# Kernel tuning notes

Measured on AMD Instinct MI355X. Metric: run time of the kernel, lower is better.

## Reference

```python
import jax, jax.numpy as jnp
import numpy as np

DIM, NH = 256, 8
B, L_INNER, L_LEAF, L_ROOT = 16, 128, 64, 16


def mha(q, k, v, wi, bi, wo, bo, nh=NH):
    # Faithful torch.nn.MultiheadAttention (batch_first): packed in_proj, q scaled by head_dim**-0.5.
    E = q.shape[-1]
    hd = E // nh
    wq, wk, wv = wi[:E], wi[E:2 * E], wi[2 * E:]
    bq, bk, bv = bi[:E], bi[E:2 * E], bi[2 * E:]

    def proj(x, w, b):
        Bx, Lx, _ = x.shape
        return (x @ w.T + b).reshape(Bx, Lx, nh, hd).transpose(0, 2, 1, 3)  # [B,H,L,hd]

    qh = proj(q, wq, bq) * (float(hd) ** -0.5)
    kh = proj(k, wk, bk)
    vh = proj(v, wv, bv)
    attn = jax.nn.softmax(jnp.einsum('bhqd,bhkd->bhqk', qh, kh), axis=-1)
    o = jnp.einsum('bhqk,bhkd->bhqd', attn, vh).transpose(0, 2, 1, 3).reshape(q.shape)
    return o @ wo.T + bo


def setup_inputs() -> dict:
    key = jax.random.key(0)
    ks = jax.random.split(key, 10)
    return {
        'leaf': jax.random.normal(ks[0], (B * L_INNER, L_LEAF, DIM), jnp.float32),
        'inner': jax.random.normal(ks[1], (B, L_INNER, DIM), jnp.float32),
        'root': jax.random.normal(ks[2], (B, L_ROOT, DIM), jnp.float32),
        'w_in': jax.random.normal(ks[3], (7, 3 * DIM, DIM), jnp.float32) * 0.02,
        'b_in': jax.random.normal(ks[4], (7, 3 * DIM), jnp.float32) * 0.02,
        'w_out': jax.random.normal(ks[5], (7, DIM, DIM), jnp.float32) * 0.02,
        'b_out': jax.random.normal(ks[6], (7, DIM), jnp.float32) * 0.02,
        'weight_leaf': jax.random.normal(ks[7], (2,), jnp.float32),
        'weight_inner': jax.random.normal(ks[8], (3,), jnp.float32),
        'weight_root': jax.random.normal(ks[9], (2,), jnp.float32),
    }


def reference(leaf, inner, root, w_in, b_in, w_out, b_out, weight_leaf, weight_inner, weight_root):
    # param slots: 0 leaf_parents, 1 leaf_siblings, 2 inner_parents, 3 inner_siblings,
    #              4 inner_children, 5 root_siblings, 6 root_children (constructed but UNUSED, as in source)
    inner_flat = inner.reshape(-1, 1, DIM)  # [B*L_inner, 1, dim]

    leaf_p = mha(leaf, inner_flat, inner_flat, w_in[0], b_in[0], w_out[0], b_out[0])
    leaf_s = mha(leaf, leaf, leaf, w_in[1], b_in[1], w_out[1], b_out[1])
    wl = jax.nn.softmax(weight_leaf)
    leaf_out = wl[0] * leaf_p + wl[1] * leaf_s

    inner_p = mha(inner, root, root, w_in[2], b_in[2], w_out[2], b_out[2])
    inner_s = mha(inner, inner, inner, w_in[3], b_in[3], w_out[3], b_out[3])
    inner_c = mha(inner_flat, leaf, leaf, w_in[4], b_in[4], w_out[4], b_out[4]).reshape(inner.shape)
    wi_ = jax.nn.softmax(weight_inner)
    inner_out = wi_[0] * inner_p + wi_[1] * inner_s + wi_[2] * inner_c

    root_s = mha(root, root, root, w_in[5], b_in[5], w_out[5], b_out[5])
    # source bug reproduced: root_c also uses attn_root_siblings (slot 5)
    root_c = mha(root, inner, inner, w_in[5], b_in[5], w_out[5], b_out[5])
    wr = jax.nn.softmax(weight_root)
    root_out = wr[0] * root_s + wr[1] * root_c

    return (leaf_out, inner_out, root_out)
```

## Files before the change

### kernel.cpp

```cpp
#include <hip/hip_runtime.h>
#include <hip/hip_bf16.h>
#include <cstdint>


#define DIM 256
#define NH 8
#define HD 32

static constexpr float SCALE = 0.17677669529663687f;

typedef __bf16 bf16x8 __attribute__((ext_vector_type(8)));
typedef __bf16 bf16x4 __attribute__((ext_vector_type(4)));
typedef float  f32x4  __attribute__((ext_vector_type(4)));

__device__ __forceinline__ float dot4(const float4 a, const float4 b) {
    return a.x * b.x + a.y * b.y + a.z * b.z + a.w * b.w;
}

__global__ __launch_bounds__(256) void cvt_f2b(const float* __restrict__ s,
                                               __bf16* __restrict__ d, int n) {
    int i = (blockIdx.x * 256 + threadIdx.x) * 4;
    if (i < n) {
        float4 v = *(const float4*)(s + i);
        d[i + 0] = (__bf16)v.x; d[i + 1] = (__bf16)v.y;
        d[i + 2] = (__bf16)v.z; d[i + 3] = (__bf16)v.w;
    }
}

__device__ void mega2_body(int g,
    const float* __restrict__ X, const float* __restrict__ inner,
    const __bf16* __restrict__ W1b, const float* __restrict__ Bi1,
    const __bf16* __restrict__ W4kvb, const float* __restrict__ W4q,
    const float* __restrict__ Bi4, __bf16* __restrict__ O1,
    float* __restrict__ Oc, char* __restrict__ smem)
{
    const int xcd  = g & 7;
    const int idx  = g >> 3;
    const int b    = xcd * 256 + (idx >> 2);
    const int hg   = idx & 3;
    const int tid  = threadIdx.x;
    const int wid  = tid >> 6;
    const int lane = tid & 63;
    const int lr   = lane & 15;
    const int lk   = (lane >> 4) * 8;
    const int prow = (lane >> 4) * 4;
    const int tok0 = wid * 16 + prow;

    __bf16* Qs  = (__bf16*)smem;
    __bf16* Ks  = (__bf16*)(smem + 9216);
    __bf16* Vt  = (__bf16*)(smem + 18432);
    __bf16* K4t = (__bf16*)(smem + 27648);
    __bf16* V4t = (__bf16*)(smem + 36864);
    __bf16* Pw  = (__bf16*)(smem + 46080 + wid * 2304);
    float* qpart = (float*)(smem + 55296);
    float* qv    = qpart + 256;
    float* psm   = qv + 64;
    float* opart = psm + 128;
    __bf16* Bs  = (__bf16*)(smem + 57600);

    bf16x8 a[8];
    {
        const float* xrow = X + ((size_t)b * 64 + wid * 16 + lr) * DIM + lk;
#pragma unroll
        for (int k = 0; k < 8; ++k) {
            float4 v0 = *(const float4*)(xrow + k * 32);
            float4 v1 = *(const float4*)(xrow + k * 32 + 4);
            bf16x8 t;
            t[0] = (__bf16)v0.x; t[1] = (__bf16)v0.y; t[2] = (__bf16)v0.z; t[3] = (__bf16)v0.w;
            t[4] = (__bf16)v1.x; t[5] = (__bf16)v1.y; t[6] = (__bf16)v1.z; t[7] = (__bf16)v1.w;
            a[k] = t;
        }
    }

    {
        const int srow = tid >> 5;
        const int scol = (tid & 31) * 8;
        auto wsrc = [&](int t) -> const __bf16* {
            if (t < 12) {
                const int sec = t >> 2, sub = t & 3;
                return W1b + (size_t)(sec * 256 + hg * 64 + sub * 16) * DIM;
            }
            const int u = t - 12, sec = u >> 2, sub = u & 3;
            return W4kvb + (size_t)(sec * 256 + hg * 64 + sub * 16) * DIM;
        };
        {
            const __bf16* p = wsrc(0);
            bf16x8 g0 = *(const bf16x8*)(p + (size_t)srow * DIM + scol);
            bf16x8 g1 = *(const bf16x8*)(p + (size_t)(8 + srow) * DIM + scol);
            *(bf16x8*)(Bs + srow * 264 + scol) = g0;
            *(bf16x8*)(Bs + (8 + srow) * 264 + scol) = g1;
        }
        __syncthreads();

        for (int t = 0; t < 20; ++t) {
            const int cur = t & 1;
            const __bf16* Bc = Bs + cur * 4224;
            bf16x8 g0, g1;
            if (t + 1 < 20) {
                const __bf16* p = wsrc(t + 1);
                g0 = *(const bf16x8*)(p + (size_t)srow * DIM + scol);
                g1 = *(const bf16x8*)(p + (size_t)(8 + srow) * DIM + scol);
            }
            f32x4 aL = {0.f, 0.f, 0.f, 0.f}, aH = {0.f, 0.f, 0.f, 0.f};
#pragma unroll
            for (int kk = 0; kk < 4; ++kk) {
                const bf16x8 bL = *(const bf16x8*)(Bc + lr * 264 + kk * 32 + lk);
                aL = __builtin_amdgcn_mfma_f32_16x16x32_bf16(a[kk], bL, aL, 0, 0, 0);
            }
#pragma unroll
            for (int kk = 0; kk < 4; ++kk) {
                const bf16x8 bH = *(const bf16x8*)(Bc + lr * 264 + (kk + 4) * 32 + lk);
                aH = __builtin_amdgcn_mfma_f32_16x16x32_bf16(a[kk + 4], bH, aH, 0, 0, 0);
            }
            const f32x4 acc = aL + aH;
            const int sub = t & 3;
            const int col = sub * 16 + lr;
            if (t < 4) {
                const float bias = Bi1[hg * 64 + sub * 16 + lr];
#pragma unroll
                for (int r = 0; r < 4; ++r)
                    Qs[(size_t)(tok0 + r) * 72 + col] = (__bf16)((acc[r] + bias) * SCALE);
            } else if (t < 8) {
                const float bias = Bi1[256 + hg * 64 + sub * 16 + lr];
#pragma unroll
                for (int r = 0; r < 4; ++r)
                    Ks[(size_t)(tok0 + r) * 72 + col] = (__bf16)(acc[r] + bias);
            } else {
                bf16x4 pv;
                if (t < 12) {
                    const float bias = Bi1[512 + hg * 64 + sub * 16 + lr];
#pragma unroll
                    for (int r = 0; r < 4; ++r) pv[r] = (__bf16)(acc[r] + bias);
                    *(bf16x4*)(Vt + (size_t)col * 72 + tok0) = pv;
                } else if (t < 16) {
                    const float bias = Bi4[256 + hg * 64 + sub * 16 + lr];
#pragma unroll
                    for (int r = 0; r < 4; ++r) pv[r] = (__bf16)(acc[r] + bias);
                    *(bf16x4*)(K4t + (size_t)col * 72 + tok0) = pv;
                } else {
                    const float bias = Bi4[512 + hg * 64 + sub * 16 + lr];
#pragma unroll
                    for (int r = 0; r < 4; ++r) pv[r] = (__bf16)(acc[r] + bias);
                    *(bf16x4*)(V4t + (size_t)col * 72 + tok0) = pv;
                }
            }
            if (t + 1 < 20) {
                __bf16* Bn = Bs + (cur ^ 1) * 4224;
                *(bf16x8*)(Bn + srow * 264 + scol) = g0;
                *(bf16x8*)(Bn + (8 + srow) * 264 + scol) = g1;
            }
            __syncthreads();
        }
    }

    {
        const int o = tid & 63, part = tid >> 6;
        const float4* wr = (const float4*)(W4q + (size_t)(hg * 64 + o) * DIM + part * 64);
        const float4* xr = (const float4*)(inner + (size_t)b * DIM + part * 64);
        float accq = 0.f;
#pragma unroll
        for (int k = 0; k < 16; ++k) accq += dot4(xr[k], wr[k]);
        qpart[part * 64 + o] = accq;
    }
    __syncthreads();

    if (tid < 64)
        qv[tid] = (qpart[tid] + qpart[64 + tid] + qpart[128 + tid] + qpart[192 + tid]
                   + Bi4[hg * 64 + tid]) * SCALE;

    const int hh = wid >> 1;
    const int qh = wid & 1;
    f32x4 s[2][4];
    {
        bf16x8 kb[4];
#pragma unroll
        for (int kt = 0; kt < 4; ++kt)
            kb[kt] = *(const bf16x8*)(Ks + (size_t)(kt * 16 + lr) * 72 + hh * 32 + lk);
#pragma unroll
        for (int q2 = 0; q2 < 2; ++q2) {
            const int qt = qh * 2 + q2;
            const bf16x8 qa = *(const bf16x8*)(Qs + (size_t)(qt * 16 + lr) * 72 + hh * 32 + lk);
#pragma unroll
            for (int kt = 0; kt < 4; ++kt) {
                f32x4 z = {0.f, 0.f, 0.f, 0.f};
                s[q2][kt] = __builtin_amdgcn_mfma_f32_16x16x32_bf16(qa, kb[kt], z, 0, 0, 0);
            }
        }
    }
#pragma unroll
    for (int q2 = 0; q2 < 2; ++q2) {
#pragma unroll
        for (int r = 0; r < 4; ++r) {
            float m = fmaxf(fmaxf(s[q2][0][r], s[q2][1][r]), fmaxf(s[q2][2][r], s[q2][3][r]));
#pragma unroll
            for (int off = 1; off < 16; off <<= 1) m = fmaxf(m, __shfl_xor(m, off));
            const float p0 = __expf(s[q2][0][r] - m), p1 = __expf(s[q2][1][r] - m);
            const float p2 = __expf(s[q2][2][r] - m), p3 = __expf(s[q2][3][r] - m);
            float t = p0 + p1 + p2 + p3;
#pragma unroll
            for (int off = 1; off < 16; off <<= 1) t += __shfl_xor(t, off);
            const float inv = 1.0f / t;
            s[q2][0][r] = p0 * inv; s[q2][1][r] = p1 * inv;
            s[q2][2][r] = p2 * inv; s[q2][3][r] = p3 * inv;
        }
    }
    {
        bf16x8 vb[2][2];
#pragma unroll
        for (int dt = 0; dt < 2; ++dt)
#pragma unroll
            for (int ks = 0; ks < 2; ++ks)
                vb[dt][ks] = *(const bf16x8*)(Vt + (size_t)(hh * 32 + dt * 16 + lr) * 72 + ks * 32 + lk);
#pragma unroll
        for (int q2 = 0; q2 < 2; ++q2) {
            const int qt = qh * 2 + q2;
#pragma unroll
            for (int kt = 0; kt < 4; ++kt)
#pragma unroll
                for (int r = 0; r < 4; ++r)
                    Pw[(size_t)(prow + r) * 72 + kt * 16 + lr] = (__bf16)s[q2][kt][r];
            bf16x8 pa[2];
#pragma unroll
            for (int ks = 0; ks < 2; ++ks)
                pa[ks] = *(const bf16x8*)(Pw + (size_t)lr * 72 + ks * 32 + lk);
#pragma unroll
            for (int dt = 0; dt < 2; ++dt) {
                f32x4 o = {0.f, 0.f, 0.f, 0.f};
#pragma unroll
                for (int ks = 0; ks < 2; ++ks)
                    o = __builtin_amdgcn_mfma_f32_16x16x32_bf16(pa[ks], vb[dt][ks], o, 0, 0, 0);
                const int colO = (hg * 2 + hh) * 32 + dt * 16 + lr;
#pragma unroll
                for (int r = 0; r < 4; ++r)
                    O1[((size_t)b * 64 + qt * 16 + prow + r) * DIM + colO] = (__bf16)o[r];
            }
        }
    }
    __syncthreads();

    if (wid < 2) {
        const int j = lane;
        float sv = 0.f;
#pragma unroll
        for (int d = 0; d < 32; ++d)
            sv += qv[wid * 32 + d] * (float)K4t[(size_t)(wid * 32 + d) * 72 + j];
        float m = sv;
#pragma unroll
        for (int off = 1; off < 64; off <<= 1) m = fmaxf(m, __shfl_xor(m, off));
        const float p = __expf(sv - m);
        float t = p;
#pragma unroll
        for (int off = 1; off < 64; off <<= 1) t += __shfl_xor(t, off);
        psm[wid * 64 + j] = p / t;
    }
    __syncthreads();

    if (tid < 128) {
        const int o = tid & 63, hf = tid >> 6;
        const int ho = o >> 5;
        float acc2 = 0.f;
#pragma unroll
        for (int j = 0; j < 32; ++j)
            acc2 += psm[ho * 64 + hf * 32 + j] * (float)V4t[(size_t)o * 72 + hf * 32 + j];
        opart[hf * 64 + o] = acc2;
    }
    __syncthreads();
    if (tid < 64)
        Oc[(size_t)b * DIM + hg * 64 + tid] = opart[tid] + opart[64 + tid];
}

__device__ void leafp_mfma_body(int bid, const float* __restrict__ inner,
    const __bf16* __restrict__ Wv0b, const __bf16* __restrict__ Wo0b,
    const float* __restrict__ b_in0, const float* __restrict__ b_out0,
    float* __restrict__ tP, char* __restrict__ smem)
{
    __bf16* tV = (__bf16*)smem;
    __bf16* Bs = (__bf16*)(smem + 33792);
    const int tid  = threadIdx.x;
    const int wid  = tid >> 6;
    const int lane = tid & 63;
    const int lr   = lane & 15;
    const int lk   = (lane >> 4) * 8;
    const int prow = (lane >> 4) * 4;
    const int tok0 = wid * 16 + prow;
    const int srow = tid >> 5;
    const int scol = (tid & 31) * 8;

    bf16x8 a[8];
    {
        const float* xrow = inner + ((size_t)bid * 64 + wid * 16 + lr) * DIM + lk;
#pragma unroll
        for (int k = 0; k < 8; ++k) {
            float4 v0 = *(const float4*)(xrow + k * 32);
            float4 v1 = *(const float4*)(xrow + k * 32 + 4);
            bf16x8 t;
            t[0] = (__bf16)v0.x; t[1] = (__bf16)v0.y; t[2] = (__bf16)v0.z; t[3] = (__bf16)v0.w;
            t[4] = (__bf16)v1.x; t[5] = (__bf16)v1.y; t[6] = (__bf16)v1.z; t[7] = (__bf16)v1.w;
            a[k] = t;
        }
    }

    {
        bf16x8 g0 = *(const bf16x8*)(Wv0b + (size_t)srow * DIM + scol);
        bf16x8 g1 = *(const bf16x8*)(Wv0b + (size_t)(8 + srow) * DIM + scol);
        *(bf16x8*)(Bs + srow * 264 + scol) = g0;
        *(bf16x8*)(Bs + (8 + srow) * 264 + scol) = g1;
    }
    __syncthreads();
    for (int t = 0; t < 16; ++t) {
        const int cur = t & 1;
        const __bf16* Bc = Bs + cur * 4224;
        bf16x8 g0, g1;
        if (t + 1 < 16) {
            const __bf16* p = Wv0b + (size_t)((t + 1) * 16) * DIM;
            g0 = *(const bf16x8*)(p + (size_t)srow * DIM + scol);
            g1 = *(const bf16x8*)(p + (size_t)(8 + srow) * DIM + scol);
        }
        f32x4 acc = {0.f, 0.f, 0.f, 0.f};
#pragma unroll
        for (int k = 0; k < 8; ++k)
            acc = __builtin_amdgcn_mfma_f32_16x16x32_bf16(
                a[k], *(const bf16x8*)(Bc + lr * 264 + k * 32 + lk), acc, 0, 0, 0);
        const float bias = b_in0[512 + t * 16 + lr];
#pragma unroll
        for (int r = 0; r < 4; ++r)
            tV[(size_t)(tok0 + r) * 264 + t * 16 + lr] = (__bf16)(acc[r] + bias);
        if (t + 1 < 16) {
            __bf16* Bn = Bs + (cur ^ 1) * 4224;
            *(bf16x8*)(Bn + srow * 264 + scol) = g0;
            *(bf16x8*)(Bn + (8 + srow) * 264 + scol) = g1;
        }
        __syncthreads();
    }

    bf16x8 a2[8];
#pragma unroll
    for (int k = 0; k < 8; ++k)
        a2[k] = *(const bf16x8*)(tV + (size_t)(wid * 16 + lr) * 264 + k * 32 + lk);
    {
        bf16x8 g0 = *(const bf16x8*)(Wo0b + (size_t)srow * DIM + scol);
        bf16x8 g1 = *(const bf16x8*)(Wo0b + (size_t)(8 + srow) * DIM + scol);
        *(bf16x8*)(Bs + srow * 264 + scol) = g0;
        *(bf16x8*)(Bs + (8 + srow) * 264 + scol) = g1;
    }
    __syncthreads();
    for (int t = 0; t < 16; ++t) {
        const int cur = t & 1;
        const __bf16* Bc = Bs + cur * 4224;
        bf16x8 g0, g1;
        if (t + 1 < 16) {
            const __bf16* p = Wo0b + (size_t)((t + 1) * 16) * DIM;
            g0 = *(const bf16x8*)(p + (size_t)srow * DIM + scol);
            g1 = *(const bf16x8*)(p + (size_t)(8 + srow) * DIM + scol);
        }
        f32x4 acc = {0.f, 0.f, 0.f, 0.f};
#pragma unroll
        for (int k = 0; k < 8; ++k)
            acc = __builtin_amdgcn_mfma_f32_16x16x32_bf16(
                a2[k], *(const bf16x8*)(Bc + lr * 264 + k * 32 + lk), acc, 0, 0, 0);
        const float bo = b_out0[t * 16 + lr];
#pragma unroll
        for (int r = 0; r < 4; ++r)
            tP[((size_t)bid * 64 + wid * 16 + prow + r) * DIM + t * 16 + lr] = acc[r] + bo;
        if (t + 1 < 16) {
            __bf16* Bn = Bs + (cur ^ 1) * 4224;
            *(bf16x8*)(Bn + srow * 264 + scol) = g0;
            *(bf16x8*)(Bn + (8 + srow) * 264 + scol) = g1;
        }
        __syncthreads();
    }
}

template <int LQ, int LK, int RQ>
__device__ void attn_body(int bx, const float* __restrict__ Xq,
                          const float* __restrict__ Xkv,
                          const float* __restrict__ Wi, const float* __restrict__ Bi,
                          float* __restrict__ O, float* __restrict__ sm)
{
    const int b   = bx >> 3;
    const int h   = bx & 7;
    const int tid = threadIdx.x;

    float* KsP = sm;
    float* VsP = KsP + LK * 33;
    float* QsP = VsP + LK * 33;
    float* SP  = QsP + LQ * 33;

    const float* xq  = Xq  + (size_t)b * LQ * DIM;
    const float* xkv = Xkv + (size_t)b * LK * DIM;

    {
        const int col   = tid & 63;
        const int which = col >> 5;
        const int d     = col & 31;
        const int row   = DIM + which * DIM + h * HD + d;
        const float4* wr = (const float4*)(Wi + (size_t)row * DIM);
        const float bias = Bi[row];
        constexpr int TT = LK / 4;
        float acc[TT];
#pragma unroll
        for (int i = 0; i < TT; ++i) acc[i] = 0.f;
        const int t0 = tid >> 6;
        for (int k4 = 0; k4 < DIM / 4; ++k4) {
            const float4 w = wr[k4];
#pragma unroll
            for (int i = 0; i < TT; ++i) {
                const int t = t0 + 4 * i;
                const float4 aa = ((const float4*)(xkv + (size_t)t * DIM))[k4];
                acc[i] += dot4(aa, w);
            }
        }
#pragma unroll
        for (int i = 0; i < TT; ++i) {
            const int t = t0 + 4 * i;
            if (which == 0) KsP[t * 33 + d] = acc[i] + bias;
            else            VsP[t * 33 + d] = acc[i] + bias;
        }
    }
    {
        constexpr int TGQ = (LQ >= 8) ? 8 : LQ;
        constexpr int TT  = LQ / TGQ;
        if (tid < 32 * TGQ) {
            const int d   = tid & 31;
            const int row = h * HD + d;
            const float4* wr = (const float4*)(Wi + (size_t)row * DIM);
            const float bias = Bi[row];
            float acc[TT];
#pragma unroll
            for (int i = 0; i < TT; ++i) acc[i] = 0.f;
            const int t0 = tid >> 5;
            for (int k4 = 0; k4 < DIM / 4; ++k4) {
                const float4 w = wr[k4];
#pragma unroll
                for (int i = 0; i < TT; ++i) {
                    const int t = t0 + TGQ * i;
                    const float4 aa = ((const float4*)(xq + (size_t)t * DIM))[k4];
                    acc[i] += dot4(aa, w);
                }
            }
#pragma unroll
            for (int i = 0; i < TT; ++i) {
                const int t = t0 + TGQ * i;
                QsP[t * 33 + d] = (acc[i] + bias) * SCALE;
            }
        }
    }
    __syncthreads();

    for (int q0 = 0; q0 < LQ; q0 += RQ) {
        for (int idx = tid; idx < RQ * LK; idx += 256) {
            const int r = idx / LK;
            const int j = idx - r * LK;
            float acc = 0.f;
#pragma unroll
            for (int d = 0; d < HD; ++d)
                acc += QsP[(q0 + r) * 33 + d] * KsP[j * 33 + d];
            SP[r * (LK + 1) + j] = acc;
        }
        __syncthreads();
        if (tid < RQ * 8) {
            const int r   = tid >> 3;
            const int sub = tid & 7;
            float m = -1e30f;
            for (int j = sub; j < LK; j += 8) m = fmaxf(m, SP[r * (LK + 1) + j]);
#pragma unroll
            for (int off = 4; off; off >>= 1) m = fmaxf(m, __shfl_xor(m, off, 8));
            float sum = 0.f;
            for (int j = sub; j < LK; j += 8) {
                const float p = __expf(SP[r * (LK + 1) + j] - m);
                SP[r * (LK + 1) + j] = p;
                sum += p;
            }
#pragma unroll
            for (int off = 4; off; off >>= 1) sum += __shfl_xor(sum, off, 8);
            const float inv = 1.0f / sum;
            for (int j = sub; j < LK; j += 8) SP[r * (LK + 1) + j] *= inv;
        }
        __syncthreads();
        for (int idx = tid; idx < RQ * HD; idx += 256) {
            const int r = idx >> 5;
            const int d = idx & 31;
            float acc = 0.f;
            for (int j = 0; j < LK; ++j)
                acc += SP[r * (LK + 1) + j] * VsP[j * 33 + d];
            O[((size_t)(b * LQ + q0 + r)) * DIM + h * HD + d] = acc;
        }
        __syncthreads();
    }
}

__global__ __launch_bounds__(256, 2) void fused_main(
    const float* __restrict__ leaf, const float* __restrict__ inner,
    const float* __restrict__ root,
    const float* __restrict__ w_in, const float* __restrict__ b_in,
    const float* __restrict__ b_out,
    const __bf16* __restrict__ W1b, const __bf16* __restrict__ W4kvb,
    const __bf16* __restrict__ Wv0b, const __bf16* __restrict__ Wo0b,
    __bf16* __restrict__ O1, float* __restrict__ Oc, float* __restrict__ tP,
    float* __restrict__ Op, float* __restrict__ Osf,
    float* __restrict__ Ors, float* __restrict__ Orc)
{
    extern __shared__ __align__(16) char smem[];
    const int bid = blockIdx.x;
    const size_t WI = 768 * 256, BI = 768;
    if (bid < 128)
        attn_body<128, 128, 16>(bid, inner, inner, w_in + 3 * WI, b_in + 3 * BI,
                                Osf, (float*)smem);
    else if (bid < 256)
        attn_body<128, 16, 32>(bid - 128, inner, root, w_in + 2 * WI, b_in + 2 * BI,
                               Op, (float*)smem);
    else if (bid < 384)
        attn_body<16, 128, 16>(bid - 256, root, inner, w_in + 5 * WI, b_in + 5 * BI,
                               Orc, (float*)smem);
    else if (bid < 512)
        attn_body<16, 16, 16>(bid - 384, root, root, w_in + 5 * WI, b_in + 5 * BI,
                              Ors, (float*)smem);
    else if (bid < 544)
        leafp_mfma_body(bid - 512, inner, Wv0b, Wo0b, b_in, b_out, tP, smem);
    else
        mega2_body(bid - 544, leaf, inner, W1b, b_in + 1 * BI, W4kvb,
                   w_in + 4 * WI, b_in + 4 * BI, O1, Oc, smem);
}

__device__ void combleaf_body(int bid, const __bf16* __restrict__ O1,
                              const __bf16* __restrict__ Wob,
                              const float* __restrict__ Bo1,
                              const float* __restrict__ tP,
                              const float* __restrict__ wleaf,
                              float* __restrict__ out, char* __restrict__ sm)
{
    const int tid  = threadIdx.x;
    const int wid  = tid >> 6;
    const int lane = tid & 63;
    const int lr   = lane & 15;
    const int lk   = (lane >> 4) * 8;
    __bf16* Bs = (__bf16*)sm;
    const int srow = tid >> 5;
    const int scol = (tid & 31) * 8;

    bf16x8 a[8];
    {
        const __bf16* ar = O1 + ((size_t)bid * 64 + wid * 16 + lr) * DIM + lk;
#pragma unroll
        for (int k = 0; k < 8; ++k) a[k] = *(const bf16x8*)(ar + k * 32);
    }
    const float e0 = __expf(wleaf[0]), e1 = __expf(wleaf[1]);
    const float wl0 = e0 / (e0 + e1), wl1 = e1 / (e0 + e1);
    const size_t row0 = (size_t)bid * 64 + wid * 16 + (lane >> 4) * 4;

    {
        bf16x8 g0 = *(const bf16x8*)(Wob + (size_t)srow * DIM + scol);
        bf16x8 g1 = *(const bf16x8*)(Wob + (size_t)(8 + srow) * DIM + scol);
        *(bf16x8*)(Bs + srow * 264 + scol) = g0;
        *(bf16x8*)(Bs + (8 + srow) * 264 + scol) = g1;
    }
    __syncthreads();

    for (int nt = 0; nt < 16; ++nt) {
        const int cur = nt & 1;
        const __bf16* Bc = Bs + cur * 4224;
        bf16x8 g0, g1;
        if (nt + 1 < 16) {
            const __bf16* p = Wob + (size_t)((nt + 1) * 16) * DIM;
            g0 = *(const bf16x8*)(p + (size_t)srow * DIM + scol);
            g1 = *(const bf16x8*)(p + (size_t)(8 + srow) * DIM + scol);
        }
        f32x4 acc = {0.f, 0.f, 0.f, 0.f};
#pragma unroll
        for (int k = 0; k < 8; ++k)
            acc = __builtin_amdgcn_mfma_f32_16x16x32_bf16(
                a[k], *(const bf16x8*)(Bc + lr * 264 + k * 32 + lk), acc, 0, 0, 0);
        const int   o  = nt * 16 + lr;
        const float bo = Bo1[o];
        const float tv = tP[(size_t)bid * DIM + o];
#pragma unroll
        for (int r = 0; r < 4; ++r)
            out[(row0 + r) * DIM + o] = wl0 * tv + wl1 * (acc[r] + bo);
        if (nt + 1 < 16) {
            __bf16* Bn = Bs + (cur ^ 1) * 4224;
            *(bf16x8*)(Bn + srow * 264 + scol) = g0;
            *(bf16x8*)(Bn + (8 + srow) * 264 + scol) = g1;
        }
        __syncthreads();
    }
}

__device__ void combine_inner_body(int vb, const float* __restrict__ Op,
    const float* __restrict__ Osf, const float* __restrict__ Oc,
    const float* __restrict__ W2, const float* __restrict__ B2,
    const float* __restrict__ W3, const float* __restrict__ B3,
    const float* __restrict__ W4, const float* __restrict__ B4,
    const float* __restrict__ winner, float* __restrict__ out, float* __restrict__ Ts)
{
    const int n0 = vb * 32;
    const int o  = threadIdx.x;
    const float e0 = __expf(winner[0]), e1 = __expf(winner[1]), e2 = __expf(winner[2]);
    const float inv = 1.f / (e0 + e1 + e2);
    const float wt0 = e0 * inv, wt1 = e1 * inv, wt2 = e2 * inv;

    float acc[32];
#pragma unroll
    for (int r = 0; r < 32; ++r) acc[r] = 0.f;
    const float biasacc = wt0 * B2[o] + wt1 * B3[o] + wt2 * B4[o];

#pragma unroll
    for (int term = 0; term < 3; ++term) {
        const float* Ob = (term == 0) ? Op : (term == 1) ? Osf : Oc;
        const float* Wb = (term == 0) ? W2 : (term == 1) ? W3 : W4;
        const float wt  = (term == 0) ? wt0 : (term == 1) ? wt1 : wt2;
        __syncthreads();
        for (int idx = threadIdx.x; idx < 32 * DIM; idx += 256)
            Ts[idx] = Ob[(size_t)n0 * DIM + idx];
        __syncthreads();
        const float4* wr = (const float4*)(Wb + (size_t)o * DIM);
        for (int k4 = 0; k4 < DIM / 4; ++k4) {
            float4 w = wr[k4];
            w.x *= wt; w.y *= wt; w.z *= wt; w.w *= wt;
#pragma unroll
            for (int r = 0; r < 32; ++r) {
                const float4 aa = *(const float4*)&Ts[r * DIM + k4 * 4];
                acc[r] += dot4(aa, w);
            }
        }
    }
#pragma unroll
    for (int r = 0; r < 32; ++r)
        out[(size_t)(n0 + r) * DIM + o] = acc[r] + biasacc;
}

__device__ void combine_root_body(int vb, const float* __restrict__ Ors,
    const float* __restrict__ Orc, const float* __restrict__ W5,
    const float* __restrict__ B5, const float* __restrict__ wroot,
    float* __restrict__ out, float* __restrict__ Ts)
{
    const int n0 = vb * 32;
    const int o  = threadIdx.x;
    const float e0 = __expf(wroot[0]), e1 = __expf(wroot[1]);
    const float w0 = e0 / (e0 + e1), w1 = e1 / (e0 + e1);
    for (int idx = threadIdx.x; idx < 32 * DIM; idx += 256)
        Ts[idx] = w0 * Ors[(size_t)n0 * DIM + idx] + w1 * Orc[(size_t)n0 * DIM + idx];
    __syncthreads();
    float acc[32];
#pragma unroll
    for (int r = 0; r < 32; ++r) acc[r] = 0.f;
    const float4* wr = (const float4*)(W5 + (size_t)o * DIM);
    for (int k4 = 0; k4 < DIM / 4; ++k4) {
        const float4 w = wr[k4];
#pragma unroll
        for (int r = 0; r < 32; ++r) {
            const float4 aa = *(const float4*)&Ts[r * DIM + k4 * 4];
            acc[r] += dot4(aa, w);
        }
    }
    const float bo = B5[o];
#pragma unroll
    for (int r = 0; r < 32; ++r)
        out[(size_t)(n0 + r) * DIM + o] = acc[r] + bo;
}

__global__ __launch_bounds__(256) void epilogue_kernel(
    const __bf16* __restrict__ O1, const __bf16* __restrict__ Wo1b,
    const float* __restrict__ w_out, const float* __restrict__ b_out,
    const float* __restrict__ tP, const float* __restrict__ Op,
    const float* __restrict__ Osf, const float* __restrict__ Oc,
    const float* __restrict__ Ors, const float* __restrict__ Orc,
    const float* __restrict__ wleaf, const float* __restrict__ winner,
    const float* __restrict__ wroot, float* __restrict__ out)
{
    extern __shared__ float smf[];
    const int bid = blockIdx.x;
    const size_t WO = 256 * 256, BO = 256;
    if (bid < 2048)
        combleaf_body(bid, O1, Wo1b, b_out + BO, tP, wleaf, out, (char*)smf);
    else if (bid < 2112)
        combine_inner_body(bid - 2048, Op, Osf, Oc,
                           w_out + 2 * WO, b_out + 2 * BO,
                           w_out + 3 * WO, b_out + 3 * BO,
                           w_out + 4 * WO, b_out + 4 * BO,
                           winner, out + 33554432, smf);
    else
        combine_root_body(bid - 2112, Ors, Orc, w_out + 5 * WO, b_out + 5 * BO,
                          wroot, out + 33554432 + 524288, smf);
}

extern "C" void kernel_launch(void* const* d_in, const int* in_sizes, int n_in,
                              void* d_out, int out_size, void* d_ws, size_t ws_size,
                              hipStream_t stream)
{
    const float* leaf   = (const float*)d_in[0];
    const float* inner  = (const float*)d_in[1];
    const float* root   = (const float*)d_in[2];
    const float* w_in   = (const float*)d_in[3];
    const float* b_in   = (const float*)d_in[4];
    const float* w_out  = (const float*)d_in[5];
    const float* b_out  = (const float*)d_in[6];
    const float* wleaf  = (const float*)d_in[7];
    const float* winner = (const float*)d_in[8];
    const float* wroot  = (const float*)d_in[9];
    float* out = (float*)d_out;

    const size_t WI = 768 * 256, WO = 256 * 256;

    char* ws = (char*)d_ws;
    __bf16* W1b   = (__bf16*)(ws);
    __bf16* W4kvb = (__bf16*)(ws + 393216);
    __bf16* Wo1b  = (__bf16*)(ws + 655360);
    __bf16* Wv0b  = (__bf16*)(ws + 786432);
    __bf16* Wo0b  = (__bf16*)(ws + 917504);
    __bf16* O1b   = (__bf16*)(ws + 1048576);
    float*  tP    = (float*)(ws + 68157440);
    float*  Oc    = (float*)(ws + 70254592);
    float*  Op    = (float*)(ws + 72351744);
    float*  Osf   = (float*)(ws + 74448896);
    float*  Ors   = (float*)(ws + 76546048);
    float*  Orc   = (float*)(ws + 76808192);

    cvt_f2b<<<192, 256, 0, stream>>>(w_in + 1 * WI, W1b, 768 * 256);
    cvt_f2b<<<128, 256, 0, stream>>>(w_in + 4 * WI + 256 * 256, W4kvb, 512 * 256);
    cvt_f2b<<<64, 256, 0, stream>>>(w_out + 1 * WO, Wo1b, 256 * 256);
    cvt_f2b<<<64, 256, 0, stream>>>(w_in + 512 * 256, Wv0b, 256 * 256);
    cvt_f2b<<<64, 256, 0, stream>>>(w_out, Wo0b, 256 * 256);

    fused_main<<<8736, 256, 74496, stream>>>(
        leaf, inner, root, w_in, b_in, b_out, W1b, W4kvb, Wv0b, Wo0b,
        O1b, Oc, tP, Op, Osf, Ors, Orc);

    epilogue_kernel<<<2120, 256, 32768, stream>>>(O1b, Wo1b, w_out, b_out, tP,
                                                  Op, Osf, Oc, Ors, Orc,
                                                  wleaf, winner, wroot, out);
}
```

Before: 728.6 us.

## Shrink fused_main shared memory by reusing buffers and raise occupancy to four blocks

The mega2 body is reorganized so the leaf-sibling attention runs right after its Q/K/V projection. Its LDS buffers are then reused for the inner-children K/V projection, and the weight staging buffer becomes single-buffered with extra barriers. This cuts dynamic shared memory from about 74KB to about 40KB, and launch bounds are raised to allow four blocks per CU. The leafp body is split into 32-row blocks with per-wave column halves, attn_body computes Q per row chunk with smaller RQ, and row strides are padded to 272/80 to avoid bank conflicts. The cost is more synchronization, no double-buffered prefetch, and tighter register limits.

```diff
diff --git a/kernel.cpp b/kernel.cpp
--- a/kernel.cpp
+++ b/kernel.cpp
@@ -47,16 +47,16 @@
     const int tok0 = wid * 16 + prow;
 
     __bf16* Qs  = (__bf16*)smem;
-    __bf16* Ks  = (__bf16*)(smem + 9216);
-    __bf16* Vt  = (__bf16*)(smem + 18432);
-    __bf16* K4t = (__bf16*)(smem + 27648);
-    __bf16* V4t = (__bf16*)(smem + 36864);
-    __bf16* Pw  = (__bf16*)(smem + 46080 + wid * 2304);
-    float* qpart = (float*)(smem + 55296);
+    __bf16* Ks  = (__bf16*)(smem + 10240);
+    __bf16* Vt  = (__bf16*)(smem + 20480);
+    __bf16* K4t = Ks;
+    __bf16* V4t = Vt;
+    __bf16* Pw  = (__bf16*)(smem + (size_t)wid * 16 * 160);
+    __bf16* Bs  = (__bf16*)(smem + 29696);
+    float* qpart = (float*)(smem + 38400);
     float* qv    = qpart + 256;
     float* psm   = qv + 64;
     float* opart = psm + 128;
-    __bf16* Bs  = (__bf16*)(smem + 57600);
 
     bf16x8 a[8];
     {
@@ -73,28 +73,163 @@
     }
 
     {
-        const int srow = tid >> 5;
-        const int scol = (tid & 31) * 8;
+        const int o = tid & 63, part = tid >> 6;
+        const float4* wr = (const float4*)(W4q + (size_t)(hg * 64 + o) * DIM + part * 64);
+        const float4* xr = (const float4*)(inner + (size_t)b * DIM + part * 64);
+        float accq = 0.f;
+#pragma unroll
+        for (int k = 0; k < 16; ++k) accq += dot4(xr[k], wr[k]);
+        qpart[part * 64 + o] = accq;
+    }
+
+    const int srow = tid >> 5;
+    const int scol = (tid & 31) * 8;
+
+    {
         auto wsrc = [&](int t) -> const __bf16* {
-            if (t < 12) {
-                const int sec = t >> 2, sub = t & 3;
-                return W1b + (size_t)(sec * 256 + hg * 64 + sub * 16) * DIM;
-            }
-            const int u = t - 12, sec = u >> 2, sub = u & 3;
-            return W4kvb + (size_t)(sec * 256 + hg * 64 + sub * 16) * DIM;
+            const int sec = t >> 2, sub = t & 3;
+            return W1b + (size_t)(sec * 256 + hg * 64 + sub * 16) * DIM;
         };
         {
             const __bf16* p = wsrc(0);
             bf16x8 g0 = *(const bf16x8*)(p + (size_t)srow * DIM + scol);
             bf16x8 g1 = *(const bf16x8*)(p + (size_t)(8 + srow) * DIM + scol);
-            *(bf16x8*)(Bs + srow * 264 + scol) = g0;
-            *(bf16x8*)(Bs + (8 + srow) * 264 + scol) = g1;
-        }
-        __syncthreads();
-
-        for (int t = 0; t < 20; ++t) {
-            const int cur = t & 1;
-            const __bf16* Bc = Bs + cur * 4224;
+            *(bf16x8*)(Bs + srow * 272 + scol) = g0;
+            *(bf16x8*)(Bs + (8 + srow) * 272 + scol) = g1;
+        }
+        __syncthreads();
+        for (int t = 0; t < 12; ++t) {
+            bf16x8 g0, g1;
+            if (t + 1 < 12) {
+                const __bf16* p = wsrc(t + 1);
+                g0 = *(const bf16x8*)(p + (size_t)srow * DIM + scol);
+                g1 = *(const bf16x8*)(p + (size_t)(8 + srow) * DIM + scol);
+            }
+            f32x4 aL = {0.f, 0.f, 0.f, 0.f}, aH = {0.f, 0.f, 0.f, 0.f};
+#pragma unroll
+            for (int kk = 0; kk < 4; ++kk) {
+                const bf16x8 bL = *(const bf16x8*)(Bs + lr * 272 + kk * 32 + lk);
+                aL = __builtin_amdgcn_mfma_f32_16x16x32_bf16(a[kk], bL, aL, 0, 0, 0);
+            }
+#pragma unroll
+            for (int kk = 0; kk < 4; ++kk) {
+                const bf16x8 bH = *(const bf16x8*)(Bs + lr * 272 + (kk + 4) * 32 + lk);
+                aH = __builtin_amdgcn_mfma_f32_16x16x32_bf16(a[kk + 4], bH, aH, 0, 0, 0);
+            }
+            const f32x4 acc = aL + aH;
+            const int sub = t & 3;
+            const int col = sub * 16 + lr;
+            if (t < 4) {
+                const float bias = Bi1[hg * 64 + sub * 16 + lr];
+#pragma unroll
+                for (int r = 0; r < 4; ++r)
+                    Qs[(size_t)(tok0 + r) * 80 + col] = (__bf16)((acc[r] + bias) * SCALE);
+            } else if (t < 8) {
+                const float bias = Bi1[256 + hg * 64 + sub * 16 + lr];
+#pragma unroll
+                for (int r = 0; r < 4; ++r)
+                    Ks[(size_t)(tok0 + r) * 80 + col] = (__bf16)(acc[r] + bias);
+            } else {
+                const float bias = Bi1[512 + hg * 64 + sub * 16 + lr];
+                bf16x4 pv;
+#pragma unroll
+                for (int r = 0; r < 4; ++r) pv[r] = (__bf16)(acc[r] + bias);
+                *(bf16x4*)(Vt + (size_t)col * 72 + tok0) = pv;
+            }
+            __syncthreads();
+            if (t + 1 < 12) {
+                *(bf16x8*)(Bs + srow * 272 + scol) = g0;
+                *(bf16x8*)(Bs + (8 + srow) * 272 + scol) = g1;
+                __syncthreads();
+            }
+        }
+    }
+    __syncthreads();
+
+    const int hh = wid >> 1;
+    const int qh = wid & 1;
+    f32x4 s[2][4];
+    {
+        bf16x8 kb[4];
+#pragma unroll
+        for (int kt = 0; kt < 4; ++kt)
+            kb[kt] = *(const bf16x8*)(Ks + (size_t)(kt * 16 + lr) * 80 + hh * 32 + lk);
+#pragma unroll
+        for (int q2 = 0; q2 < 2; ++q2) {
+            const int qt = qh * 2 + q2;
+            const bf16x8 qa = *(const bf16x8*)(Qs + (size_t)(qt * 16 + lr) * 80 + hh * 32 + lk);
+#pragma unroll
+            for (int kt = 0; kt < 4; ++kt) {
+                f32x4 z = {0.f, 0.f, 0.f, 0.f};
+                s[q2][kt] = __builtin_amdgcn_mfma_f32_16x16x32_bf16(qa, kb[kt], z, 0, 0, 0);
+            }
+        }
+    }
+#pragma unroll
+    for (int q2 = 0; q2 < 2; ++q2) {
+#pragma unroll
+        for (int r = 0; r < 4; ++r) {
+            float m = fmaxf(fmaxf(s[q2][0][r], s[q2][1][r]), fmaxf(s[q2][2][r], s[q2][3][r]));
+#pragma unroll
+            for (int off = 1; off < 16; off <<= 1) m = fmaxf(m, __shfl_xor(m, off));
+            const float p0 = __expf(s[q2][0][r] - m), p1 = __expf(s[q2][1][r] - m);
+            const float p2 = __expf(s[q2][2][r] - m), p3 = __expf(s[q2][3][r] - m);
+            float t = p0 + p1 + p2 + p3;
+#pragma unroll
+            for (int off = 1; off < 16; off <<= 1) t += __shfl_xor(t, off);
+            const float inv = 1.0f / t;
+            s[q2][0][r] = p0 * inv; s[q2][1][r] = p1 * inv;
+            s[q2][2][r] = p2 * inv; s[q2][3][r] = p3 * inv;
+        }
+    }
+    bf16x8 vb[2][2];
+#pragma unroll
+    for (int dt = 0; dt < 2; ++dt)
+#pragma unroll
+        for (int ks = 0; ks < 2; ++ks)
+            vb[dt][ks] = *(const bf16x8*)(Vt + (size_t)(hh * 32 + dt * 16 + lr) * 72 + ks * 32 + lk);
+    __syncthreads();
+
+#pragma unroll
+    for (int q2 = 0; q2 < 2; ++q2) {
+        const int qt = qh * 2 + q2;
+#pragma unroll
+        for (int kt = 0; kt < 4; ++kt)
+#pragma unroll
+            for (int r = 0; r < 4; ++r)
+                Pw[(size_t)(prow + r) * 80 + kt * 16 + lr] = (__bf16)s[q2][kt][r];
+        bf16x8 pa[2];
+#pragma unroll
+        for (int ks = 0; ks < 2; ++ks)
+            pa[ks] = *(const bf16x8*)(Pw + (size_t)lr * 80 + ks * 32 + lk);
+#pragma unroll
+        for (int dt = 0; dt < 2; ++dt) {
+            f32x4 o = {0.f, 0.f, 0.f, 0.f};
+#pragma unroll
+            for (int ks = 0; ks < 2; ++ks)
+                o = __builtin_amdgcn_mfma_f32_16x16x32_bf16(pa[ks], vb[dt][ks], o, 0, 0, 0);
+            const int colO = (hg * 2 + hh) * 32 + dt * 16 + lr;
+#pragma unroll
+            for (int r = 0; r < 4; ++r)
+                O1[((size_t)b * 64 + qt * 16 + prow + r) * DIM + colO] = (__bf16)o[r];
+        }
+    }
+
+    {
+        auto wsrc = [&](int t) -> const __bf16* {
+            const int u = t - 12, sec = u >> 2, sub = t & 3;
+            return W4kvb + (size_t)(sec * 256 + hg * 64 + sub * 16) * DIM;
+        };
+        {
+            const __bf16* p = wsrc(12);
+            bf16x8 g0 = *(const bf16x8*)(p + (size_t)srow * DIM + scol);
+            bf16x8 g1 = *(const bf16x8*)(p + (size_t)(8 + srow) * DIM + scol);
+            __syncthreads();
+            *(bf16x8*)(Bs + srow * 272 + scol) = g0;
+            *(bf16x8*)(Bs + (8 + srow) * 272 + scol) = g1;
+        }
+        __syncthreads();
+        for (int t = 12; t < 20; ++t) {
             bf16x8 g0, g1;
             if (t + 1 < 20) {
                 const __bf16* p = wsrc(t + 1);
@@ -104,138 +239,41 @@
             f32x4 aL = {0.f, 0.f, 0.f, 0.f}, aH = {0.f, 0.f, 0.f, 0.f};
 #pragma unroll
             for (int kk = 0; kk < 4; ++kk) {
-                const bf16x8 bL = *(const bf16x8*)(Bc + lr * 264 + kk * 32 + lk);
+                const bf16x8 bL = *(const bf16x8*)(Bs + lr * 272 + kk * 32 + lk);
                 aL = __builtin_amdgcn_mfma_f32_16x16x32_bf16(a[kk], bL, aL, 0, 0, 0);
             }
 #pragma unroll
             for (int kk = 0; kk < 4; ++kk) {
-                const bf16x8 bH = *(const bf16x8*)(Bc + lr * 264 + (kk + 4) * 32 + lk);
+                const bf16x8 bH = *(const bf16x8*)(Bs + lr * 272 + (kk + 4) * 32 + lk);
                 aH = __builtin_amdgcn_mfma_f32_16x16x32_bf16(a[kk + 4], bH, aH, 0, 0, 0);
             }
             const f32x4 acc = aL + aH;
             const int sub = t & 3;
             const int col = sub * 16 + lr;
-            if (t < 4) {
-                const float bias = Bi1[hg * 64 + sub * 16 + lr];
-#pragma unroll
-                for (int r = 0; r < 4; ++r)
-                    Qs[(size_t)(tok0 + r) * 72 + col] = (__bf16)((acc[r] + bias) * SCALE);
-            } else if (t < 8) {
-                const float bias = Bi1[256 + hg * 64 + sub * 16 + lr];
-#pragma unroll
-                for (int r = 0; r < 4; ++r)
-                    Ks[(size_t)(tok0 + r) * 72 + col] = (__bf16)(acc[r] + bias);
+            bf16x4 pv;
+            if (t < 16) {
+                const float bias = Bi4[256 + hg * 64 + sub * 16 + lr];
+#pragma unroll
+                for (int r = 0; r < 4; ++r) pv[r] = (__bf16)(acc[r] + bias);
+                *(bf16x4*)(K4t + (size_t)col * 80 + tok0) = pv;
             } else {
-                bf16x4 pv;
-                if (t < 12) {
-                    const float bias = Bi1[512 + hg * 64 + sub * 16 + lr];
-#pragma unroll
-                    for (int r = 0; r < 4; ++r) pv[r] = (__bf16)(acc[r] + bias);
-                    *(bf16x4*)(Vt + (size_t)col * 72 + tok0) = pv;
-                } else if (t < 16) {
-                    const float bias = Bi4[256 + hg * 64 + sub * 16 + lr];
-#pragma unroll
-                    for (int r = 0; r < 4; ++r) pv[r] = (__bf16)(acc[r] + bias);
-                    *(bf16x4*)(K4t + (size_t)col * 72 + tok0) = pv;
-                } else {
-                    const float bias = Bi4[512 + hg * 64 + sub * 16 + lr];
-#pragma unroll
-                    for (int r = 0; r < 4; ++r) pv[r] = (__bf16)(acc[r] + bias);
-                    *(bf16x4*)(V4t + (size_t)col * 72 + tok0) = pv;
-                }
-            }
+                const float bias = Bi4[512 + hg * 64 + sub * 16 + lr];
+#pragma unroll
+                for (int r = 0; r < 4; ++r) pv[r] = (__bf16)(acc[r] + bias);
+                *(bf16x4*)(V4t + (size_t)col * 72 + tok0) = pv;
+            }
+            __syncthreads();
             if (t + 1 < 20) {
-                __bf16* Bn = Bs + (cur ^ 1) * 4224;
-                *(bf16x8*)(Bn + srow * 264 + scol) = g0;
-                *(bf16x8*)(Bn + (8 + srow) * 264 + scol) = g1;
-            }
-            __syncthreads();
-        }
-    }
-
-    {
-        const int o = tid & 63, part = tid >> 6;
-        const float4* wr = (const float4*)(W4q + (size_t)(hg * 64 + o) * DIM + part * 64);
-        const float4* xr = (const float4*)(inner + (size_t)b * DIM + part * 64);
-        float accq = 0.f;
-#pragma unroll
-        for (int k = 0; k < 16; ++k) accq += dot4(xr[k], wr[k]);
-        qpart[part * 64 + o] = accq;
-    }
-    __syncthreads();
+                *(bf16x8*)(Bs + srow * 272 + scol) = g0;
+                *(bf16x8*)(Bs + (8 + srow) * 272 + scol) = g1;
+                __syncthreads();
+            }
+        }
+    }
 
     if (tid < 64)
         qv[tid] = (qpart[tid] + qpart[64 + tid] + qpart[128 + tid] + qpart[192 + tid]
                    + Bi4[hg * 64 + tid]) * SCALE;
-
-    const int hh = wid >> 1;
-    const int qh = wid & 1;
-    f32x4 s[2][4];
-    {
-        bf16x8 kb[4];
-#pragma unroll
-        for (int kt = 0; kt < 4; ++kt)
-            kb[kt] = *(const bf16x8*)(Ks + (size_t)(kt * 16 + lr) * 72 + hh * 32 + lk);
-#pragma unroll
-        for (int q2 = 0; q2 < 2; ++q2) {
-            const int qt = qh * 2 + q2;
-            const bf16x8 qa = *(const bf16x8*)(Qs + (size_t)(qt * 16 + lr) * 72 + hh * 32 + lk);
-#pragma unroll
-            for (int kt = 0; kt < 4; ++kt) {
-                f32x4 z = {0.f, 0.f, 0.f, 0.f};
-                s[q2][kt] = __builtin_amdgcn_mfma_f32_16x16x32_bf16(qa, kb[kt], z, 0, 0, 0);
-            }
-        }
-    }
-#pragma unroll
-    for (int q2 = 0; q2 < 2; ++q2) {
-#pragma unroll
-        for (int r = 0; r < 4; ++r) {
-            float m = fmaxf(fmaxf(s[q2][0][r], s[q2][1][r]), fmaxf(s[q2][2][r], s[q2][3][r]));
-#pragma unroll
-            for (int off = 1; off < 16; off <<= 1) m = fmaxf(m, __shfl_xor(m, off));
-            const float p0 = __expf(s[q2][0][r] - m), p1 = __expf(s[q2][1][r] - m);
-            const float p2 = __expf(s[q2][2][r] - m), p3 = __expf(s[q2][3][r] - m);
-            float t = p0 + p1 + p2 + p3;
-#pragma unroll
-            for (int off = 1; off < 16; off <<= 1) t += __shfl_xor(t, off);
-            const float inv = 1.0f / t;
-            s[q2][0][r] = p0 * inv; s[q2][1][r] = p1 * inv;
-            s[q2][2][r] = p2 * inv; s[q2][3][r] = p3 * inv;
-        }
-    }
-    {
-        bf16x8 vb[2][2];
-#pragma unroll
-        for (int dt = 0; dt < 2; ++dt)
-#pragma unroll
-            for (int ks = 0; ks < 2; ++ks)
-                vb[dt][ks] = *(const bf16x8*)(Vt + (size_t)(hh * 32 + dt * 16 + lr) * 72 + ks * 32 + lk);
-#pragma unroll
-        for (int q2 = 0; q2 < 2; ++q2) {
-            const int qt = qh * 2 + q2;
-#pragma unroll
-            for (int kt = 0; kt < 4; ++kt)
-#pragma unroll
-                for (int r = 0; r < 4; ++r)
-                    Pw[(size_t)(prow + r) * 72 + kt * 16 + lr] = (__bf16)s[q2][kt][r];
-            bf16x8 pa[2];
-#pragma unroll
-            for (int ks = 0; ks < 2; ++ks)
-                pa[ks] = *(const bf16x8*)(Pw + (size_t)lr * 72 + ks * 32 + lk);
-#pragma unroll
-            for (int dt = 0; dt < 2; ++dt) {
-                f32x4 o = {0.f, 0.f, 0.f, 0.f};
-#pragma unroll
-                for (int ks = 0; ks < 2; ++ks)
-                    o = __builtin_amdgcn_mfma_f32_16x16x32_bf16(pa[ks], vb[dt][ks], o, 0, 0, 0);
-                const int colO = (hg * 2 + hh) * 32 + dt * 16 + lr;
-#pragma unroll
-                for (int r = 0; r < 4; ++r)
-                    O1[((size_t)b * 64 + qt * 16 + prow + r) * DIM + colO] = (__bf16)o[r];
-            }
-        }
-    }
     __syncthreads();
 
     if (wid < 2) {
@@ -243,7 +281,7 @@
         float sv = 0.f;
 #pragma unroll
         for (int d = 0; d < 32; ++d)
-            sv += qv[wid * 32 + d] * (float)K4t[(size_t)(wid * 32 + d) * 72 + j];
+            sv += qv[wid * 32 + d] * (float)K4t[(size_t)(wid * 32 + d) * 80 + j];
         float m = sv;
 #pragma unroll
         for (int off = 1; off < 64; off <<= 1) m = fmaxf(m, __shfl_xor(m, off));
@@ -275,20 +313,22 @@
     float* __restrict__ tP, char* __restrict__ smem)
 {
     __bf16* tV = (__bf16*)smem;
-    __bf16* Bs = (__bf16*)(smem + 33792);
     const int tid  = threadIdx.x;
     const int wid  = tid >> 6;
     const int lane = tid & 63;
     const int lr   = lane & 15;
     const int lk   = (lane >> 4) * 8;
     const int prow = (lane >> 4) * 4;
-    const int tok0 = wid * 16 + prow;
-    const int srow = tid >> 5;
-    const int scol = (tid & 31) * 8;
+    const int rg   = wid & 1;
+    const int ch   = wid >> 1;
+    __bf16* Bsc = (__bf16*)(smem + 16896 + ch * 8704);
+    const int l    = tid & 127;
+    const int brow = l >> 3;
+    const int bcol = (l & 7) * 32;
 
     bf16x8 a[8];
     {
-        const float* xrow = inner + ((size_t)bid * 64 + wid * 16 + lr) * DIM + lk;
+        const float* xrow = inner + ((size_t)bid * 32 + rg * 16 + lr) * DIM + lk;
 #pragma unroll
         for (int k = 0; k < 8; ++k) {
             float4 v0 = *(const float4*)(xrow + k * 32);
@@ -300,74 +340,51 @@
         }
     }
 
-    {
-        bf16x8 g0 = *(const bf16x8*)(Wv0b + (size_t)srow * DIM + scol);
-        bf16x8 g1 = *(const bf16x8*)(Wv0b + (size_t)(8 + srow) * DIM + scol);
-        *(bf16x8*)(Bs + srow * 264 + scol) = g0;
-        *(bf16x8*)(Bs + (8 + srow) * 264 + scol) = g1;
-    }
-    __syncthreads();
-    for (int t = 0; t < 16; ++t) {
-        const int cur = t & 1;
-        const __bf16* Bc = Bs + cur * 4224;
-        bf16x8 g0, g1;
-        if (t + 1 < 16) {
-            const __bf16* p = Wv0b + (size_t)((t + 1) * 16) * DIM;
-            g0 = *(const bf16x8*)(p + (size_t)srow * DIM + scol);
-            g1 = *(const bf16x8*)(p + (size_t)(8 + srow) * DIM + scol);
-        }
+    auto stage_tile = [&](const __bf16* W, int t) {
+        const __bf16* p = W + (size_t)(t * 16 + brow) * DIM + bcol;
+#pragma unroll
+        for (int q = 0; q < 4; ++q)
+            *(bf16x8*)(Bsc + brow * 272 + bcol + q * 8) = *(const bf16x8*)(p + q * 8);
+    };
+
+    stage_tile(Wv0b, ch * 8);
+    __syncthreads();
+    for (int i = 0; i < 8; ++i) {
+        const int t = ch * 8 + i;
         f32x4 acc = {0.f, 0.f, 0.f, 0.f};
 #pragma unroll
         for (int k = 0; k < 8; ++k)
             acc = __builtin_amdgcn_mfma_f32_16x16x32_bf16(
-                a[k], *(const bf16x8*)(Bc + lr * 264 + k * 32 + lk), acc, 0, 0, 0);
+                a[k], *(const bf16x8*)(Bsc + lr * 272 + k * 32 + lk), acc, 0, 0, 0);
         const float bias = b_in0[512 + t * 16 + lr];
 #pragma unroll
         for (int r = 0; r < 4; ++r)
-            tV[(size_t)(tok0 + r) * 264 + t * 16 + lr] = (__bf16)(acc[r] + bias);
-        if (t + 1 < 16) {
-            __bf16* Bn = Bs + (cur ^ 1) * 4224;
-            *(bf16x8*)(Bn + srow * 264 + scol) = g0;
-            *(bf16x8*)(Bn + (8 + srow) * 264 + scol) = g1;
-        }
-        __syncthreads();
-    }
+            tV[(size_t)(rg * 16 + prow + r) * 264 + t * 16 + lr] = (__bf16)(acc[r] + bias);
+        __syncthreads();
+        if (i + 1 < 8) { stage_tile(Wv0b, t + 1); __syncthreads(); }
+    }
+    __syncthreads();
 
     bf16x8 a2[8];
 #pragma unroll
     for (int k = 0; k < 8; ++k)
-        a2[k] = *(const bf16x8*)(tV + (size_t)(wid * 16 + lr) * 264 + k * 32 + lk);
-    {
-        bf16x8 g0 = *(const bf16x8*)(Wo0b + (size_t)srow * DIM + scol);
-        bf16x8 g1 = *(const bf16x8*)(Wo0b + (size_t)(8 + srow) * DIM + scol);
-        *(bf16x8*)(Bs + srow * 264 + scol) = g0;
-        *(bf16x8*)(Bs + (8 + srow) * 264 + scol) = g1;
-    }
-    __syncthreads();
-    for (int t = 0; t < 16; ++t) {
-        const int cur = t & 1;
-        const __bf16* Bc = Bs + cur * 4224;
-        bf16x8 g0, g1;
-        if (t + 1 < 16) {
-            const __bf16* p = Wo0b + (size_t)((t + 1) * 16) * DIM;
-            g0 = *(const bf16x8*)(p + (size_t)srow * DIM + scol);
-            g1 = *(const bf16x8*)(p + (size_t)(8 + srow) * DIM + scol);
-        }
+        a2[k] = *(const bf16x8*)(tV + (size_t)(rg * 16 + lr) * 264 + k * 32 + lk);
+    __syncthreads();
+    stage_tile(Wo0b, ch * 8);
+    __syncthreads();
+    for (int i = 0; i < 8; ++i) {
+        const int t = ch * 8 + i;
         f32x4 acc = {0.f, 0.f, 0.f, 0.f};
 #pragma unroll
         for (int k = 0; k < 8; ++k)
             acc = __builtin_amdgcn_mfma_f32_16x16x32_bf16(
-                a2[k], *(const bf16x8*)(Bc + lr * 264 + k * 32 + lk), acc, 0, 0, 0);
+                a2[k], *(const bf16x8*)(Bsc + lr * 272 + k * 32 + lk), acc, 0, 0, 0);
         const float bo = b_out0[t * 16 + lr];
 #pragma unroll
         for (int r = 0; r < 4; ++r)
-            tP[((size_t)bid * 64 + wid * 16 + prow + r) * DIM + t * 16 + lr] = acc[r] + bo;
-        if (t + 1 < 16) {
-            __bf16* Bn = Bs + (cur ^ 1) * 4224;
-            *(bf16x8*)(Bn + srow * 264 + scol) = g0;
-            *(bf16x8*)(Bn + (8 + srow) * 264 + scol) = g1;
-        }
-        __syncthreads();
+            tP[((size_t)bid * 32 + rg * 16 + prow + r) * DIM + t * 16 + lr] = acc[r] + bo;
+        __syncthreads();
+        if (i + 1 < 8) { stage_tile(Wo0b, t + 1); __syncthreads(); }
     }
 }
 
@@ -384,7 +401,7 @@
     float* KsP = sm;
     float* VsP = KsP + LK * 33;
     float* QsP = VsP + LK * 33;
-    float* SP  = QsP + LQ * 33;
+    float* SP  = QsP + RQ * 33;
 
     const float* xq  = Xq  + (size_t)b * LQ * DIM;
     const float* xkv = Xkv + (size_t)b * LK * DIM;
@@ -417,44 +434,32 @@
             else            VsP[t * 33 + d] = acc[i] + bias;
         }
     }
-    {
-        constexpr int TGQ = (LQ >= 8) ? 8 : LQ;
-        constexpr int TT  = LQ / TGQ;
-        if (tid < 32 * TGQ) {
-            const int d   = tid & 31;
+    __syncthreads();
+
+    for (int q0 = 0; q0 < LQ; q0 += RQ) {
+        {
+            const int d  = tid & 31;
+            const int rg = tid >> 5;
             const int row = h * HD + d;
             const float4* wr = (const float4*)(Wi + (size_t)row * DIM);
             const float bias = Bi[row];
-            float acc[TT];
-#pragma unroll
-            for (int i = 0; i < TT; ++i) acc[i] = 0.f;
-            const int t0 = tid >> 5;
-            for (int k4 = 0; k4 < DIM / 4; ++k4) {
-                const float4 w = wr[k4];
-#pragma unroll
-                for (int i = 0; i < TT; ++i) {
-                    const int t = t0 + TGQ * i;
-                    const float4 aa = ((const float4*)(xq + (size_t)t * DIM))[k4];
-                    acc[i] += dot4(aa, w);
-                }
-            }
-#pragma unroll
-            for (int i = 0; i < TT; ++i) {
-                const int t = t0 + TGQ * i;
-                QsP[t * 33 + d] = (acc[i] + bias) * SCALE;
-            }
-        }
-    }
-    __syncthreads();
-
-    for (int q0 = 0; q0 < LQ; q0 += RQ) {
+#pragma unroll
+            for (int i = 0; i < RQ / 8; ++i) {
+                const int rloc = rg + 8 * i;
+                float acc = 0.f;
+                const float4* xr = (const float4*)(xq + (size_t)(q0 + rloc) * DIM);
+                for (int k4 = 0; k4 < DIM / 4; ++k4) acc += dot4(xr[k4], wr[k4]);
+                QsP[rloc * 33 + d] = (acc + bias) * SCALE;
+            }
+        }
+        __syncthreads();
         for (int idx = tid; idx < RQ * LK; idx += 256) {
             const int r = idx / LK;
             const int j = idx - r * LK;
             float acc = 0.f;
 #pragma unroll
             for (int d = 0; d < HD; ++d)
-                acc += QsP[(q0 + r) * 33 + d] * KsP[j * 33 + d];
+                acc += QsP[r * 33 + d] * KsP[j * 33 + d];
             SP[r * (LK + 1) + j] = acc;
         }
         __syncthreads();
@@ -489,7 +494,7 @@
     }
 }
 
-__global__ __launch_bounds__(256, 2) void fused_main(
+__global__ __launch_bounds__(256, 4) void fused_main(
     const float* __restrict__ leaf, const float* __restrict__ inner,
     const float* __restrict__ root,
     const float* __restrict__ w_in, const float* __restrict__ b_in,
@@ -504,21 +509,21 @@
     const int bid = blockIdx.x;
     const size_t WI = 768 * 256, BI = 768;
     if (bid < 128)
-        attn_body<128, 128, 16>(bid, inner, inner, w_in + 3 * WI, b_in + 3 * BI,
-                                Osf, (float*)smem);
+        attn_body<128, 128, 8>(bid, inner, inner, w_in + 3 * WI, b_in + 3 * BI,
+                               Osf, (float*)smem);
     else if (bid < 256)
-        attn_body<128, 16, 32>(bid - 128, inner, root, w_in + 2 * WI, b_in + 2 * BI,
+        attn_body<16, 128, 8>(bid - 128, root, inner, w_in + 5 * WI, b_in + 5 * BI,
+                              Orc, (float*)smem);
+    else if (bid < 384)
+        attn_body<128, 16, 32>(bid - 256, inner, root, w_in + 2 * WI, b_in + 2 * BI,
                                Op, (float*)smem);
-    else if (bid < 384)
-        attn_body<16, 128, 16>(bid - 256, root, inner, w_in + 5 * WI, b_in + 5 * BI,
-                               Orc, (float*)smem);
     else if (bid < 512)
         attn_body<16, 16, 16>(bid - 384, root, root, w_in + 5 * WI, b_in + 5 * BI,
                               Ors, (float*)smem);
-    else if (bid < 544)
+    else if (bid < 576)
         leafp_mfma_body(bid - 512, inner, Wv0b, Wo0b, b_in, b_out, tP, smem);
     else
-        mega2_body(bid - 544, leaf, inner, W1b, b_in + 1 * BI, W4kvb,
+        mega2_body(bid - 576, leaf, inner, W1b, b_in + 1 * BI, W4kvb,
                    w_in + 4 * WI, b_in + 4 * BI, O1, Oc, smem);
 }
 
@@ -551,14 +556,14 @@
     {
         bf16x8 g0 = *(const bf16x8*)(Wob + (size_t)srow * DIM + scol);
         bf16x8 g1 = *(const bf16x8*)(Wob + (size_t)(8 + srow) * DIM + scol);
-        *(bf16x8*)(Bs + srow * 264 + scol) = g0;
-        *(bf16x8*)(Bs + (8 + srow) * 264 + scol) = g1;
+        *(bf16x8*)(Bs + srow * 272 + scol) = g0;
+        *(bf16x8*)(Bs + (8 + srow) * 272 + scol) = g1;
     }
     __syncthreads();
 
     for (int nt = 0; nt < 16; ++nt) {
         const int cur = nt & 1;
-        const __bf16* Bc = Bs + cur * 4224;
+        const __bf16* Bc = Bs + cur * 4352;
         bf16x8 g0, g1;
         if (nt + 1 < 16) {
             const __bf16* p = Wob + (size_t)((nt + 1) * 16) * DIM;
@@ -569,7 +574,7 @@
 #pragma unroll
         for (int k = 0; k < 8; ++k)
             acc = __builtin_amdgcn_mfma_f32_16x16x32_bf16(
-                a[k], *(const bf16x8*)(Bc + lr * 264 + k * 32 + lk), acc, 0, 0, 0);
+                a[k], *(const bf16x8*)(Bc + lr * 272 + k * 32 + lk), acc, 0, 0, 0);
         const int   o  = nt * 16 + lr;
         const float bo = Bo1[o];
         const float tv = tP[(size_t)bid * DIM + o];
@@ -577,9 +582,9 @@
         for (int r = 0; r < 4; ++r)
             out[(row0 + r) * DIM + o] = wl0 * tv + wl1 * (acc[r] + bo);
         if (nt + 1 < 16) {
-            __bf16* Bn = Bs + (cur ^ 1) * 4224;
-            *(bf16x8*)(Bn + srow * 264 + scol) = g0;
-            *(bf16x8*)(Bn + (8 + srow) * 264 + scol) = g1;
+            __bf16* Bn = Bs + (cur ^ 1) * 4352;
+            *(bf16x8*)(Bn + srow * 272 + scol) = g0;
+            *(bf16x8*)(Bn + (8 + srow) * 272 + scol) = g1;
         }
         __syncthreads();
     }
@@ -721,7 +726,7 @@
     cvt_f2b<<<64, 256, 0, stream>>>(w_in + 512 * 256, Wv0b, 256 * 256);
     cvt_f2b<<<64, 256, 0, stream>>>(w_out, Wo0b, 256 * 256);
 
-    fused_main<<<8736, 256, 74496, stream>>>(
+    fused_main<<<8768, 256, 40704, stream>>>(
         leaf, inner, root, w_in, b_in, b_out, W1b, W4kvb, Wv0b, Wo0b,
         O1b, Oc, tP, Op, Osf, Ors, Orc);
 
```

Result: slower. 927.2 us (+27.3%).
